# Performance work log

Hardware: AMD Instinct MI355X
Metric: run time of the kernel (lower is better)

## Reference

```python
import jax, jax.numpy as jnp
import numpy as np

DEPTH = 12
N_FEATURES = 512
BATCH = 16384
N_NODES = 2 ** DEPTH - 1   # 4095 internal nodes, concatenated level-by-level
N_LEAVES = 2 ** DEPTH      # 4096


def setup_inputs() -> dict:
    key = jax.random.key(0)
    k_x, k_w, k_b, k_s, k_l = jax.random.split(key, 5)
    x_input = jax.random.normal(k_x, (BATCH, N_FEATURES), dtype=jnp.float32)
    # Per-level Linear(n_features, 2**d) weights concatenated on the output dim:
    # level d occupies rows [2**d - 1, 2**(d+1) - 1).
    bound = 1.0 / np.sqrt(N_FEATURES)  # torch Linear default init scale
    W_all = jax.random.uniform(k_w, (N_NODES, N_FEATURES), dtype=jnp.float32,
                               minval=-bound, maxval=bound)
    b_all = jax.random.uniform(k_b, (N_NODES,), dtype=jnp.float32,
                               minval=-bound, maxval=bound)
    # original uses max(randn, 1) -> positive steepness >= 1
    s_all = jax.random.uniform(k_s, (N_NODES,), dtype=jnp.float32,
                               minval=1.0, maxval=2.0)
    leaves = jax.random.normal(k_l, (N_LEAVES,), dtype=jnp.float32)
    return {"x_input": x_input, "W_all": W_all, "b_all": b_all,
            "s_all": s_all, "leaves": leaves}


def reference(x_input, W_all, b_all, s_all, leaves):
    B = x_input.shape[0]
    # One fused GEMM for all depth levels: [B, 2**depth - 1]
    logits = x_input @ W_all.T + b_all
    p_all = jax.nn.sigmoid(logits * s_all)
    # Recursive path-probability product down the binary tree.
    # out[:, j] at level d is the prob of reaching child j (j = 2*node + side),
    # matching the original dict insertion order (node ascending, left then right).
    out = jnp.ones((B, 1), dtype=p_all.dtype)
    for d in range(DEPTH):
        start = 2 ** d - 1
        p = p_all[:, start:start + 2 ** d]          # [B, 2**d]
        # interleave left (parent*p) and right (parent*(1-p)) children
        out = jnp.stack([out * p, out * (1.0 - p)], axis=-1).reshape(B, 2 ** (d + 1))
    # weighted sum over leaves
    return (jax.nn.sigmoid(leaves) * out).sum(axis=1)   # [B]
```

## Files before the change

### kernel.cpp

```cpp
#include <hip/hip_runtime.h>
#include <hip/hip_bf16.h>

#define M_DIM   16384
#define K_DIM   512
#define NNODES  4095
#define NPERM   4096
#define NTOP    128
#define NWROWS  (NPERM + NTOP)

#define NBOT_BLOCKS (64 * 32)
#define NTOT_BLOCKS (NBOT_BLOCKS + 64)
#define BUFB    24576
#define PT_STRIDE 135
#define SLF_OFF (256 * PT_STRIDE * 2)
#define SMEM_BYTES (SLF_OFF + 512)

typedef __bf16   bf16x8 __attribute__((ext_vector_type(8)));
typedef float    floatx4 __attribute__((ext_vector_type(4)));

__device__ __forceinline__ float sigmoidf_(float z) {
    return __builtin_amdgcn_rcpf(1.f + __expf(-z));
}

__device__ __forceinline__ void gld_lds16(const void* g, void* l) {
    __builtin_amdgcn_global_load_lds(
        (const __attribute__((address_space(1))) void*)g,
        (__attribute__((address_space(3))) void*)l, 16, 0, 0);
}

__global__ __launch_bounds__(256) void cvt_all(const float* __restrict__ X,
                                               const float* __restrict__ W,
                                               const float* __restrict__ bias,
                                               const float* __restrict__ scale,
                                               __hip_bfloat16* __restrict__ Xb,
                                               __hip_bfloat16* __restrict__ Wb,
                                               float* __restrict__ bp,
                                               float* __restrict__ sp) {
    const int bid = blockIdx.x;
    if (bid < 4096) {
        const int idx = (bid * 256 + threadIdx.x) * 8;
        float4 f0 = *reinterpret_cast<const float4*>(X + idx);
        float4 f1 = *reinterpret_cast<const float4*>(X + idx + 4);
        __hip_bfloat16 h[8];
        h[0] = __float2bfloat16(f0.x); h[1] = __float2bfloat16(f0.y);
        h[2] = __float2bfloat16(f0.z); h[3] = __float2bfloat16(f0.w);
        h[4] = __float2bfloat16(f1.x); h[5] = __float2bfloat16(f1.y);
        h[6] = __float2bfloat16(f1.z); h[7] = __float2bfloat16(f1.w);
        *reinterpret_cast<int4*>(Xb + idx) = *reinterpret_cast<int4*>(h);
        return;
    }
    const int idx = ((bid - 4096) * 256 + threadIdx.x) * 8;
    const int r = idx >> 9;
    const int k = idx & 511;
    int node;
    if (r < NPERM) {
        const int t = r >> 5, o = r & 31;
        int d, q;
        if (o < 16)       { d = 11; q = o; }
        else if (o < 24)  { d = 10; q = o - 16; }
        else if (o < 28)  { d = 9;  q = o - 24; }
        else if (o < 30)  { d = 8;  q = o - 28; }
        else if (o == 30) { d = 7;  q = 0; }
        else              { d = -1; q = 0; }
        node = (d < 0) ? -1 : ((1 << d) - 1 + (t << (d - 7)) + q);
    } else {
        const int c = r - NPERM;
        node = (c < 127) ? c : -1;
    }
    __hip_bfloat16 h[8];
    if (node >= 0) {
        const float* src = W + (size_t)node * 512 + k;
        float4 f0 = *reinterpret_cast<const float4*>(src);
        float4 f1 = *reinterpret_cast<const float4*>(src + 4);
        h[0] = __float2bfloat16(f0.x); h[1] = __float2bfloat16(f0.y);
        h[2] = __float2bfloat16(f0.z); h[3] = __float2bfloat16(f0.w);
        h[4] = __float2bfloat16(f1.x); h[5] = __float2bfloat16(f1.y);
        h[6] = __float2bfloat16(f1.z); h[7] = __float2bfloat16(f1.w);
    } else {
        #pragma unroll
        for (int i = 0; i < 8; ++i) h[i] = __float2bfloat16(0.f);
    }
    *reinterpret_cast<int4*>(Wb + idx) = *reinterpret_cast<int4*>(h);
    if (k == 0) {
        bp[r] = (node >= 0) ? bias[node]  : 0.f;
        sp[r] = (node >= 0) ? scale[node] : 1.f;
    }
}

__global__ __launch_bounds__(256, 2) void gemm_fold(
    const __hip_bfloat16* __restrict__ A,
    const __hip_bfloat16* __restrict__ B,
    const float* __restrict__ bp,
    const float* __restrict__ sp,
    const float* __restrict__ leaves,
    float* __restrict__ partial,
    _Float16* __restrict__ ptop)
{
    __shared__ char smem[SMEM_BYTES] __attribute__((aligned(16)));
    _Float16* pt  = (_Float16*)smem;
    float*    slf = (float*)(smem + SLF_OFF);

    const int tid  = threadIdx.x;
    const int lane = tid & 63;
    const int wv   = tid >> 6;
    const int bid  = blockIdx.x;
    int tile_m, tile_n;
    if (bid < NBOT_BLOCKS) { tile_m = bid >> 5; tile_n = bid & 31; }
    else                   { tile_m = bid - NBOT_BLOCKS; tile_n = 32; }
    const int m0 = tile_m * 256;
    const int n0 = tile_n * 128;

    if (tile_n < 32 && tid < 128) slf[tid] = sigmoidf_(leaves[n0 + tid]);

    const int wvm = wv >> 1;
    const int wvn = wv & 1;
    const int quad = lane >> 4;
    const int l15  = lane & 15;

    const int lrow2 = l15 >> 1;
    const int psE   = ((((l15 & 1) << 2) | quad) ^ lrow2) * 8;

    const int lidx  = (lane & 7) ^ (lane >> 3);
    const int gsrow = 2 * (lane >> 3) + ((lidx >> 2) & 1);
    const int swz   = (lidx & 3) * 16;
    const char* gAp[4];
    const char* gBp[2];
    char* sA[4];
    char* sB[2];
    #pragma unroll
    for (int c = 0; c < 4; ++c) {
        const int rbase = c * 64 + wv * 16;
        gAp[c] = (const char*)(A + (size_t)(m0 + rbase + gsrow) * K_DIM) + swz;
        sA[c]  = smem + rbase * 64;
    }
    #pragma unroll
    for (int c = 0; c < 2; ++c) {
        const int rbase = c * 64 + wv * 16;
        gBp[c] = (const char*)(B + (size_t)(n0 + rbase + gsrow) * K_DIM) + swz;
        sB[c]  = smem + 16384 + rbase * 64;
    }

    floatx4 acc[8][4];
    #pragma unroll
    for (int i = 0; i < 8; ++i)
        #pragma unroll
        for (int j = 0; j < 4; ++j)
            acc[i][j] = (floatx4){0.f, 0.f, 0.f, 0.f};

    #pragma unroll
    for (int c = 0; c < 4; ++c) { gld_lds16(gAp[c], sA[c]); gAp[c] += 64; }
    #pragma unroll
    for (int c = 0; c < 2; ++c) { gld_lds16(gBp[c], sB[c]); gBp[c] += 64; }

    #pragma unroll 1
    for (int k0 = 0; k0 < 16; ++k0) {
        __syncthreads();
        if (k0 < 15) {
            const int boff = ((k0 + 1) & 1) * BUFB;
            #pragma unroll
            for (int c = 0; c < 4; ++c) { gld_lds16(gAp[c], sA[c] + boff); gAp[c] += 64; }
            #pragma unroll
            for (int c = 0; c < 2; ++c) { gld_lds16(gBp[c], sB[c] + boff); gBp[c] += 64; }
        }
        const __hip_bfloat16* cA =
            (const __hip_bfloat16*)(smem + (k0 & 1) * BUFB);
        const __hip_bfloat16* cB = cA + 8192;

        bf16x8 bfr[4];
        #pragma unroll
        for (int j = 0; j < 4; ++j)
            bfr[j] = *reinterpret_cast<const bf16x8*>(
                &cB[(wvn * 32 + j * 8 + lrow2) * 64 + psE]);
        #pragma unroll
        for (int i = 0; i < 8; ++i) {
            const bf16x8 af = *reinterpret_cast<const bf16x8*>(
                &cA[(wvm * 64 + i * 8 + lrow2) * 64 + psE]);
            #pragma unroll
            for (int j = 0; j < 4; ++j)
                acc[i][j] = __builtin_amdgcn_mfma_f32_16x16x32_bf16(
                    af, bfr[j], acc[i][j], 0, 0, 0);
        }
    }
    __syncthreads();

    float bn[4], sn[4];
    #pragma unroll
    for (int j = 0; j < 4; ++j) {
        const int n = n0 + wvn * 64 + j * 16 + l15;
        bn[j] = bp[n];
        sn[j] = sp[n];
    }

    if (tile_n == 32) {
        #pragma unroll
        for (int i = 0; i < 8; ++i) {
            #pragma unroll
            for (int r = 0; r < 4; ++r) {
                const int m = m0 + wvm * 128 + i * 16 + quad * 4 + r;
                #pragma unroll
                for (int j = 0; j < 4; ++j) {
                    const int col = wvn * 64 + j * 16 + l15;
                    ptop[(size_t)m * 128 + col] =
                        (_Float16)sigmoidf_((acc[i][j][r] + bn[j]) * sn[j]);
                }
            }
        }
        return;
    }

    #pragma unroll
    for (int i = 0; i < 8; ++i) {
        #pragma unroll
        for (int r = 0; r < 4; ++r) {
            const int row = wvm * 128 + i * 16 + quad * 4 + r;
            #pragma unroll
            for (int j = 0; j < 4; ++j) {
                const int col = wvn * 64 + j * 16 + l15;
                pt[row * PT_STRIDE + col] =
                    (_Float16)sigmoidf_((acc[i][j][r] + bn[j]) * sn[j]);
            }
        }
    }
    __syncthreads();

    #pragma unroll
    for (int z = 0; z < 4; ++z) {
        const int task = tid + z * 256;
        const int row  = task >> 2;
        const int st   = task & 3;
        const _Float16* pp = pt + row * PT_STRIDE + st * 32;
        const float*    sl = slf + st * 32;
        float v[16];
        #pragma unroll
        for (int q = 0; q < 16; ++q) {
            const float p = (float)pp[q];
            v[q] = p * sl[2 * q] + (1.f - p) * sl[2 * q + 1];
        }
        #pragma unroll
        for (int q = 0; q < 8; ++q) {
            const float p = (float)pp[16 + q];
            v[q] = p * v[2 * q] + (1.f - p) * v[2 * q + 1];
        }
        #pragma unroll
        for (int q = 0; q < 4; ++q) {
            const float p = (float)pp[24 + q];
            v[q] = p * v[2 * q] + (1.f - p) * v[2 * q + 1];
        }
        #pragma unroll
        for (int q = 0; q < 2; ++q) {
            const float p = (float)pp[28 + q];
            v[q] = p * v[2 * q] + (1.f - p) * v[2 * q + 1];
        }
        const float p7 = (float)pp[30];
        partial[(size_t)(m0 + row) * 128 + tile_n * 4 + st] =
            p7 * v[0] + (1.f - p7) * v[1];
    }
}

__global__ __launch_bounds__(256) void final_fold(
    const float* __restrict__ partial,
    const _Float16* __restrict__ ptop,
    float* __restrict__ out)
{
    __shared__ float    pL[64 * 129];
    __shared__ _Float16 pq[64 * 134];

    const int tid = threadIdx.x;
    const int m0  = blockIdx.x * 64;

    #pragma unroll
    for (int it = 0; it < 32; ++it) {
        const int idx = tid + it * 256;
        const int row = idx >> 7;
        const int c   = idx & 127;
        pL[row * 129 + c] = partial[(size_t)(m0 + row) * 128 + c];
        pq[row * 134 + c] = ptop[(size_t)(m0 + row) * 128 + c];
    }
    __syncthreads();

    if (tid < 64) {
        float* v = pL + tid * 129;
        const _Float16* pr = pq + tid * 134;
        #pragma unroll
        for (int d = 6; d >= 1; --d) {
            const int base = (1 << d) - 1;
            const int cnt  = 1 << d;
            for (int q = 0; q < cnt; ++q) {
                const float p = (float)pr[base + q];
                v[q] = p * v[2 * q] + (1.f - p) * v[2 * q + 1];
            }
        }
        const float p0 = (float)pr[0];
        out[m0 + tid] = p0 * v[0] + (1.f - p0) * v[1];
    }
}

__global__ __launch_bounds__(256) void tnn_fallback(
    const float* __restrict__ X, const float* __restrict__ W,
    const float* __restrict__ bias, const float* __restrict__ scale,
    const float* __restrict__ leaves, float* __restrict__ out)
{
    __shared__ float xr[512];
    __shared__ float sl[4096];
    __shared__ float pp[4096];
    __shared__ float v0[2048];
    __shared__ float v1[1024];
    const int tid  = threadIdx.x;
    const int lane = tid & 63;
    const int wv   = tid >> 6;
    const int b    = blockIdx.x;
    for (int i = tid; i < 512;  i += 256) xr[i] = X[(size_t)b * 512 + i];
    for (int i = tid; i < 4096; i += 256) sl[i] = sigmoidf_(leaves[i]);
    __syncthreads();
    for (int n = wv; n < NNODES; n += 4) {
        float sum = 0.f;
        const float* wr = W + (size_t)n * 512;
        for (int k = lane; k < 512; k += 64) sum += xr[k] * wr[k];
        #pragma unroll
        for (int off = 32; off; off >>= 1) sum += __shfl_xor(sum, off);
        if (lane == 0) pp[n] = sigmoidf_((sum + bias[n]) * scale[n]);
    }
    __syncthreads();
    for (int j = tid; j < 2048; j += 256) {
        const float p = pp[2047 + j];
        v0[j] = p * sl[2 * j] + (1.f - p) * sl[2 * j + 1];
    }
    __syncthreads();
    float* src = v0;
    float* dst = v1;
    for (int d = 10; d >= 0; --d) {
        const int width = 1 << d;
        const int start = width - 1;
        for (int j = tid; j < width; j += 256) {
            const float p = pp[start + j];
            dst[j] = p * src[2 * j] + (1.f - p) * src[2 * j + 1];
        }
        __syncthreads();
        float* t = src; src = dst; dst = t;
    }
    if (tid == 0) out[b] = src[0];
}

extern "C" void kernel_launch(void* const* d_in, const int* in_sizes, int n_in,
                              void* d_out, int out_size, void* d_ws, size_t ws_size,
                              hipStream_t stream) {
    const float* X      = (const float*)d_in[0];
    const float* W      = (const float*)d_in[1];
    const float* bias   = (const float*)d_in[2];
    const float* scale  = (const float*)d_in[3];
    const float* leaves = (const float*)d_in[4];
    float* out = (float*)d_out;

    const size_t offX  = 0;
    const size_t offW  = (size_t)M_DIM * K_DIM * 2;
    const size_t offB  = offW + (size_t)NWROWS * K_DIM * 2;
    const size_t offS  = offB + (size_t)NWROWS * 4;
    const size_t offP  = offS + (size_t)NWROWS * 4;
    const size_t offT  = offP + (size_t)M_DIM * 128 * 4;
    const size_t need  = offT + (size_t)M_DIM * 128 * 2;

    if (ws_size >= need) {
        __hip_bfloat16* Xb = (__hip_bfloat16*)((char*)d_ws + offX);
        __hip_bfloat16* Wb = (__hip_bfloat16*)((char*)d_ws + offW);
        float* bp = (float*)((char*)d_ws + offB);
        float* sp = (float*)((char*)d_ws + offS);
        float* partial = (float*)((char*)d_ws + offP);
        _Float16* ptop = (_Float16*)((char*)d_ws + offT);
        cvt_all<<<4096 + 1056, 256, 0, stream>>>(X, W, bias, scale, Xb, Wb, bp, sp);
        gemm_fold<<<NTOT_BLOCKS, 256, 0, stream>>>(
            Xb, Wb, bp, sp, leaves, partial, ptop);
        final_fold<<<M_DIM / 64, 256, 0, stream>>>(partial, ptop, out);
    } else {
        tnn_fallback<<<M_DIM, 256, 0, stream>>>(X, W, bias, scale, leaves, out);
    }
}
```

Before: 197.3 us.

## Enlarge GEMM tile to 256x256 with 512 threads and triple-buffered LDS ring

Doubles the N tile to 256 columns and uses 8 waves per block, so each block now folds 8 subtrees of depth 5. The two-buffer LDS scheme becomes a three-slot ring with a K step of 64, staged global-to-LDS loads, split barriers, explicit waitcnts and raised priority around the MFMA phases. This is meant to raise operand reuse per LDS byte and hide load latency better. W padding grows to 4352 rows so the top-level tile fits the wider N tiling. The cost is more LDS per block, which may lower occupancy.

```diff
diff --git a/kernel.cpp b/kernel.cpp
--- a/kernel.cpp
+++ b/kernel.cpp
@@ -7,13 +7,15 @@
 #define NPERM   4096
 #define NTOP    128
 #define NWROWS  (NPERM + NTOP)
-
-#define NBOT_BLOCKS (64 * 32)
+#define NWPAD   4352
+
+#define NBOT_BLOCKS (64 * 16)
 #define NTOT_BLOCKS (NBOT_BLOCKS + 64)
-#define BUFB    24576
-#define PT_STRIDE 135
+#define SLOTB   32768
+#define RING3   (3 * SLOTB)
+#define PT_STRIDE 263
 #define SLF_OFF (256 * PT_STRIDE * 2)
-#define SMEM_BYTES (SLF_OFF + 512)
+#define SMEM_BYTES (SLF_OFF + 1024)
 
 typedef __bf16   bf16x8 __attribute__((ext_vector_type(8)));
 typedef float    floatx4 __attribute__((ext_vector_type(4)));
@@ -87,7 +89,7 @@
     }
 }
 
-__global__ __launch_bounds__(256, 2) void gemm_fold(
+__global__ __launch_bounds__(512, 2) void gemm_fold(
     const __hip_bfloat16* __restrict__ A,
     const __hip_bfloat16* __restrict__ B,
     const float* __restrict__ bp,
@@ -105,40 +107,33 @@
     const int wv   = tid >> 6;
     const int bid  = blockIdx.x;
     int tile_m, tile_n;
-    if (bid < NBOT_BLOCKS) { tile_m = bid >> 5; tile_n = bid & 31; }
-    else                   { tile_m = bid - NBOT_BLOCKS; tile_n = 32; }
+    if (bid < NBOT_BLOCKS) { tile_m = bid >> 4; tile_n = bid & 15; }
+    else                   { tile_m = bid - NBOT_BLOCKS; tile_n = 16; }
     const int m0 = tile_m * 256;
-    const int n0 = tile_n * 128;
-
-    if (tile_n < 32 && tid < 128) slf[tid] = sigmoidf_(leaves[n0 + tid]);
-
-    const int wvm = wv >> 1;
-    const int wvn = wv & 1;
+    const int n0 = tile_n * 256;
+
+    if (tile_n < 16 && tid < 256) slf[tid] = sigmoidf_(leaves[n0 + tid]);
+
+    const int wvm = wv >> 2;
+    const int wvn = wv & 3;
     const int quad = lane >> 4;
     const int l15  = lane & 15;
-
     const int lrow2 = l15 >> 1;
-    const int psE   = ((((l15 & 1) << 2) | quad) ^ lrow2) * 8;
+    const int psB   = (((((l15 & 1) << 2) | quad) ^ lrow2) * 16);
 
     const int lidx  = (lane & 7) ^ (lane >> 3);
     const int gsrow = 2 * (lane >> 3) + ((lidx >> 2) & 1);
     const int swz   = (lidx & 3) * 16;
-    const char* gAp[4];
+
+    const char* gAp[2];
     const char* gBp[2];
-    char* sA[4];
-    char* sB[2];
-    #pragma unroll
-    for (int c = 0; c < 4; ++c) {
-        const int rbase = c * 64 + wv * 16;
+    #pragma unroll
+    for (int c = 0; c < 2; ++c) {
+        const int rbase = c * 128 + wv * 16;
         gAp[c] = (const char*)(A + (size_t)(m0 + rbase + gsrow) * K_DIM) + swz;
-        sA[c]  = smem + rbase * 64;
-    }
-    #pragma unroll
-    for (int c = 0; c < 2; ++c) {
-        const int rbase = c * 64 + wv * 16;
         gBp[c] = (const char*)(B + (size_t)(n0 + rbase + gsrow) * K_DIM) + swz;
-        sB[c]  = smem + 16384 + rbase * 64;
-    }
+    }
+    const int ldsoff = wv * 1024;
 
     floatx4 acc[8][4];
     #pragma unroll
@@ -148,38 +143,80 @@
             acc[i][j] = (floatx4){0.f, 0.f, 0.f, 0.f};
 
     #pragma unroll
-    for (int c = 0; c < 4; ++c) { gld_lds16(gAp[c], sA[c]); gAp[c] += 64; }
-    #pragma unroll
-    for (int c = 0; c < 2; ++c) { gld_lds16(gBp[c], sB[c]); gBp[c] += 64; }
-
+    for (int c = 0; c < 2; ++c) { gld_lds16(gAp[c], smem + c * 8192 + ldsoff);            gAp[c] += 64; }
+    #pragma unroll
+    for (int c = 0; c < 2; ++c) { gld_lds16(gBp[c], smem + 16384 + c * 8192 + ldsoff);    gBp[c] += 64; }
+    #pragma unroll
+    for (int c = 0; c < 2; ++c) { gld_lds16(gAp[c], smem + SLOTB + c * 8192 + ldsoff);          gAp[c] += 64; }
+    #pragma unroll
+    for (int c = 0; c < 2; ++c) { gld_lds16(gBp[c], smem + SLOTB + 16384 + c * 8192 + ldsoff);  gBp[c] += 64; }
+    asm volatile("s_waitcnt vmcnt(4)" ::: "memory");
+    __builtin_amdgcn_s_barrier();
+
+    int cur = 0;
+    int stg = 2 * SLOTB;
     #pragma unroll 1
-    for (int k0 = 0; k0 < 16; ++k0) {
-        __syncthreads();
-        if (k0 < 15) {
-            const int boff = ((k0 + 1) & 1) * BUFB;
-            #pragma unroll
-            for (int c = 0; c < 4; ++c) { gld_lds16(gAp[c], sA[c] + boff); gAp[c] += 64; }
-            #pragma unroll
-            for (int c = 0; c < 2; ++c) { gld_lds16(gBp[c], sB[c] + boff); gBp[c] += 64; }
-        }
-        const __hip_bfloat16* cA =
-            (const __hip_bfloat16*)(smem + (k0 & 1) * BUFB);
-        const __hip_bfloat16* cB = cA + 8192;
-
-        bf16x8 bfr[4];
+    for (int kt = 0; kt < 16; ++kt) {
+        const char* cAb = smem + cur;
+        const char* cBb = cAb + 16384;
+
+        bf16x8 bfr[4], af[4];
         #pragma unroll
         for (int j = 0; j < 4; ++j)
             bfr[j] = *reinterpret_cast<const bf16x8*>(
-                &cB[(wvn * 32 + j * 8 + lrow2) * 64 + psE]);
-        #pragma unroll
-        for (int i = 0; i < 8; ++i) {
-            const bf16x8 af = *reinterpret_cast<const bf16x8*>(
-                &cA[(wvm * 64 + i * 8 + lrow2) * 64 + psE]);
+                cBb + (wvn * 32 + j * 8 + lrow2) * 128 + psB);
+        #pragma unroll
+        for (int i = 0; i < 4; ++i)
+            af[i] = *reinterpret_cast<const bf16x8*>(
+                cAb + (wvm * 64 + i * 8 + lrow2) * 128 + psB);
+        if (kt < 14) {
+            gld_lds16(gAp[0], smem + stg + ldsoff);
+            gld_lds16(gAp[1], smem + stg + 8192 + ldsoff);
+            gAp[0] += 64; gAp[1] += 64;
+        }
+        __builtin_amdgcn_s_barrier();
+        asm volatile("s_waitcnt lgkmcnt(0)" ::: "memory");
+        __builtin_amdgcn_sched_barrier(0);
+        __builtin_amdgcn_s_setprio(1);
+        #pragma unroll
+        for (int i = 0; i < 4; ++i)
             #pragma unroll
             for (int j = 0; j < 4; ++j)
                 acc[i][j] = __builtin_amdgcn_mfma_f32_16x16x32_bf16(
-                    af, bfr[j], acc[i][j], 0, 0, 0);
-        }
+                    af[i], bfr[j], acc[i][j], 0, 0, 0);
+        __builtin_amdgcn_s_setprio(0);
+
+        bf16x8 af2[4];
+        #pragma unroll
+        for (int i = 0; i < 4; ++i)
+            af2[i] = *reinterpret_cast<const bf16x8*>(
+                cAb + (wvm * 64 + 32 + i * 8 + lrow2) * 128 + psB);
+        if (kt < 14) {
+            gld_lds16(gBp[0], smem + stg + 16384 + ldsoff);
+            gld_lds16(gBp[1], smem + stg + 24576 + ldsoff);
+            gBp[0] += 64; gBp[1] += 64;
+        }
+        __builtin_amdgcn_s_barrier();
+        asm volatile("s_waitcnt lgkmcnt(0)" ::: "memory");
+        __builtin_amdgcn_sched_barrier(0);
+        __builtin_amdgcn_s_setprio(1);
+        #pragma unroll
+        for (int i = 0; i < 4; ++i)
+            #pragma unroll
+            for (int j = 0; j < 4; ++j)
+                acc[i + 4][j] = __builtin_amdgcn_mfma_f32_16x16x32_bf16(
+                    af2[i], bfr[j], acc[i + 4][j], 0, 0, 0);
+        __builtin_amdgcn_s_setprio(0);
+
+        if (kt < 14) {
+            asm volatile("s_waitcnt vmcnt(4)" ::: "memory");
+        } else {
+            asm volatile("s_waitcnt vmcnt(0)" ::: "memory");
+        }
+        __builtin_amdgcn_s_barrier();
+
+        cur = (cur == 2 * SLOTB) ? 0 : cur + SLOTB;
+        stg = (stg == 2 * SLOTB) ? 0 : stg + SLOTB;
     }
     __syncthreads();
 
@@ -191,17 +228,19 @@
         sn[j] = sp[n];
     }
 
-    if (tile_n == 32) {
-        #pragma unroll
-        for (int i = 0; i < 8; ++i) {
+    if (tile_n == 16) {
+        if (wvn < 2) {
             #pragma unroll
-            for (int r = 0; r < 4; ++r) {
-                const int m = m0 + wvm * 128 + i * 16 + quad * 4 + r;
+            for (int i = 0; i < 8; ++i) {
                 #pragma unroll
-                for (int j = 0; j < 4; ++j) {
-                    const int col = wvn * 64 + j * 16 + l15;
-                    ptop[(size_t)m * 128 + col] =
-                        (_Float16)sigmoidf_((acc[i][j][r] + bn[j]) * sn[j]);
+                for (int r = 0; r < 4; ++r) {
+                    const int m = m0 + wvm * 128 + i * 16 + quad * 4 + r;
+                    #pragma unroll
+                    for (int j = 0; j < 4; ++j) {
+                        const int col = wvn * 64 + j * 16 + l15;
+                        ptop[(size_t)m * 128 + col] =
+                            (_Float16)sigmoidf_((acc[i][j][r] + bn[j]) * sn[j]);
+                    }
                 }
             }
         }
@@ -225,9 +264,9 @@
 
     #pragma unroll
     for (int z = 0; z < 4; ++z) {
-        const int task = tid + z * 256;
-        const int row  = task >> 2;
-        const int st   = task & 3;
+        const int task = tid + z * 512;
+        const int row  = task >> 3;
+        const int st   = task & 7;
         const _Float16* pp = pt + row * PT_STRIDE + st * 32;
         const float*    sl = slf + st * 32;
         float v[16];
@@ -252,7 +291,7 @@
             v[q] = p * v[2 * q] + (1.f - p) * v[2 * q + 1];
         }
         const float p7 = (float)pp[30];
-        partial[(size_t)(m0 + row) * 128 + tile_n * 4 + st] =
+        partial[(size_t)(m0 + row) * 128 + tile_n * 8 + st] =
             p7 * v[0] + (1.f - p7) * v[1];
     }
 }
@@ -353,9 +392,9 @@
 
     const size_t offX  = 0;
     const size_t offW  = (size_t)M_DIM * K_DIM * 2;
-    const size_t offB  = offW + (size_t)NWROWS * K_DIM * 2;
-    const size_t offS  = offB + (size_t)NWROWS * 4;
-    const size_t offP  = offS + (size_t)NWROWS * 4;
+    const size_t offB  = offW + (size_t)NWPAD * K_DIM * 2;
+    const size_t offS  = offB + (size_t)NWPAD * 4;
+    const size_t offP  = offS + (size_t)NWPAD * 4;
     const size_t offT  = offP + (size_t)M_DIM * 128 * 4;
     const size_t need  = offT + (size_t)M_DIM * 128 * 2;
 
@@ -366,8 +405,8 @@
         float* sp = (float*)((char*)d_ws + offS);
         float* partial = (float*)((char*)d_ws + offP);
         _Float16* ptop = (_Float16*)((char*)d_ws + offT);
-        cvt_all<<<4096 + 1056, 256, 0, stream>>>(X, W, bias, scale, Xb, Wb, bp, sp);
-        gemm_fold<<<NTOT_BLOCKS, 256, 0, stream>>>(
+        cvt_all<<<4096 + 1088, 256, 0, stream>>>(X, W, bias, scale, Xb, Wb, bp, sp);
+        gemm_fold<<<NTOT_BLOCKS, 512, 0, stream>>>(
             Xb, Wb, bp, sp, leaves, partial, ptop);
         final_fold<<<M_DIM / 64, 256, 0, stream>>>(partial, ptop, out);
     } else {
```

Measured after the change: 228.5 us. 15.9% more time.
